# Performance work log

Measured on AMD Instinct MI355X. Metric: run time of the kernel, lower is better.

The kernel has to match this reference:

```python
import jax, jax.numpy as jnp
import numpy as np

B, T, C, H = 2, 2048, 1024, 16
D = C // H  # head_dim = 64

def setup_inputs() -> dict:
    key = jax.random.key(0)
    ks = jax.random.split(key, 9)
    s = 1.0 / np.sqrt(C)
    return {
        "x": jax.random.normal(ks[0], (B, T, C), dtype=jnp.float32),
        "Wq": jax.random.uniform(ks[1], (C, C), jnp.float32, -s, s),
        "bq": jax.random.uniform(ks[2], (C,), jnp.float32, -s, s),
        "Wk": jax.random.uniform(ks[3], (C, C), jnp.float32, -s, s),
        "bk": jax.random.uniform(ks[4], (C,), jnp.float32, -s, s),
        "Wv": jax.random.uniform(ks[5], (C, C), jnp.float32, -s, s),
        "bv": jax.random.uniform(ks[6], (C,), jnp.float32, -s, s),
        "Wp": jax.random.uniform(ks[7], (C, C), jnp.float32, -s, s),
        "bp": jax.random.uniform(ks[8], (C,), jnp.float32, -s, s),
    }

def reference(x, Wq, bq, Wk, bk, Wv, bv, Wp, bp):
    # Linear layers: torch nn.Linear weight is [out,in], so x @ W.T + b
    q = x @ Wq.T + bq
    k = x @ Wk.T + bk
    v = x @ Wv.T + bv
    # [B,T,C] -> [B,H,T,D]
    q = q.reshape(B, T, H, D).transpose(0, 2, 1, 3)
    k = k.reshape(B, T, H, D).transpose(0, 2, 1, 3)
    v = v.reshape(B, T, H, D).transpose(0, 2, 1, 3)
    att = jnp.einsum("bhqd,bhkd->bhqk", q, k) / jnp.sqrt(jnp.float32(D))
    causal = jnp.tril(jnp.ones((T, T), dtype=bool))  # [T,T]
    att = jnp.where(causal, att, jnp.float32(-jnp.inf))
    att = jax.nn.softmax(att, axis=-1)
    out = jnp.einsum("bhqk,bhkd->bhqd", att, v)
    out = out.transpose(0, 2, 1, 3).reshape(B, T, C)
    return out @ Wp.T + bp
```

## Files before the change

kernel.cpp:

```cpp
#include <hip/hip_runtime.h>
#include <hip/hip_bf16.h>
#include <stdint.h>

typedef __bf16 bf16x8 __attribute__((ext_vector_type(8)));
typedef __bf16 bf16x4 __attribute__((ext_vector_type(4)));
typedef __bf16 bf16x2 __attribute__((ext_vector_type(2)));
typedef float  f32x4  __attribute__((ext_vector_type(4)));
typedef float  f32x16v __attribute__((ext_vector_type(16)));

#define MFMA16(A,B,Cc) __builtin_amdgcn_mfma_f32_16x16x32_bf16(A,B,Cc,0,0,0)
#define MFMA32(A,B,Cc) __builtin_amdgcn_mfma_f32_32x32x16_bf16(A,B,Cc,0,0,0)

__device__ inline unsigned pack2(float a, float b) {
  union { bf16x2 v; unsigned u; } t;
  t.v[0] = (__bf16)a; t.v[1] = (__bf16)b;
  return t.u;
}
__device__ inline bf16x8 frag4(unsigned w0, unsigned w1, unsigned w2, unsigned w3) {
  union { unsigned u[4]; bf16x8 v; } t;
  t.u[0] = w0; t.u[1] = w1; t.u[2] = w2; t.u[3] = w3;
  return t.v;
}

__device__ inline void pswap(unsigned& a, unsigned& b) {
#if __has_builtin(__builtin_amdgcn_permlane32_swap)
  auto r = __builtin_amdgcn_permlane32_swap(a, b, false, false);
  a = r[0]; b = r[1];
#else
  asm volatile("v_permlane32_swap_b32 %0, %1" : "+v"(a), "+v"(b));
#endif
}
__device__ inline float cross32_sum(float v) {
  unsigned a = __builtin_bit_cast(unsigned, v), b = a;
  pswap(a, b);
  return __builtin_bit_cast(float, a) + __builtin_bit_cast(float, b);
}

__device__ inline void gl16(const __bf16* g, __bf16* l) {
  __builtin_amdgcn_global_load_lds(
      (const __attribute__((address_space(1))) void*)(uintptr_t)g,
      (__attribute__((address_space(3))) void*)(uintptr_t)l, 16, 0, 0);
}

__global__ __launch_bounds__(256) void conv_kernel(
    const float* __restrict__ x,
    const float* __restrict__ Wq, const float* __restrict__ Wk,
    const float* __restrict__ Wv, const float* __restrict__ Wp,
    __bf16* __restrict__ xb, __bf16* __restrict__ Wb)
{
  const int z = blockIdx.y;
  const float* src;
  __bf16* dst;
  int n4;
  if (z == 0) { src = x;  dst = xb; n4 = 1048576; }
  else {
    src = (z == 1) ? Wq : (z == 2) ? Wk : (z == 3) ? Wv : Wp;
    dst = Wb + (size_t)(z - 1) * 1048576;
    n4  = 262144;
  }
  const f32x4* s4 = (const f32x4*)src;
  for (int i = blockIdx.x * 256 + threadIdx.x; i < n4; i += gridDim.x * 256) {
    const f32x4 v = s4[i];
    bf16x4 o;
#pragma unroll
    for (int j = 0; j < 4; ++j) o[j] = (__bf16)v[j];
    *(bf16x4*)(dst + (size_t)i * 4) = o;
  }
}

__device__ inline void gemm_core(const __bf16* __restrict__ A,
                                 const __bf16* __restrict__ W,
                                 int m0, int n0,
                                 __bf16* As, __bf16* Bs,
                                 f32x4 (&acc)[4][4])
{
  const int tid = threadIdx.x, lane = tid & 63;
  const int wid = tid >> 6, wr = wid >> 1, wc = wid & 1;
  const int g = lane >> 4, cl = lane & 15;
  const int sr = tid >> 2, sk = (tid & 3) * 8;
  __bf16* AsW = As + (tid & 192) * 8;
  __bf16* BsW = Bs + (tid & 192) * 8;

  for (int k0 = 0; k0 < 1024; k0 += 32) {
    __syncthreads();
    gl16(A + (size_t)(m0 + sr)      * 1024 + k0 + sk, AsW);
    gl16(A + (size_t)(m0 + sr + 64) * 1024 + k0 + sk, AsW + 2048);
    gl16(W + (size_t)(n0 + sr)      * 1024 + k0 + sk, BsW);
    gl16(W + (size_t)(n0 + sr + 64) * 1024 + k0 + sk, BsW + 2048);
    __syncthreads();
    bf16x8 af[4], bfr[4];
#pragma unroll
    for (int m = 0; m < 4; ++m)
      af[m] = *(const bf16x8*)(As + (wr * 64 + m * 16 + cl) * 32 + g * 8);
#pragma unroll
    for (int n = 0; n < 4; ++n)
      bfr[n] = *(const bf16x8*)(Bs + (wc * 64 + n * 16 + cl) * 32 + g * 8);
#pragma unroll
    for (int m = 0; m < 4; ++m)
#pragma unroll
      for (int n = 0; n < 4; ++n)
        acc[m][n] = MFMA16(af[m], bfr[n], acc[m][n]);
  }
}

__global__ __launch_bounds__(256) void gemm_qkv128(
    const __bf16* __restrict__ xb, const __bf16* __restrict__ Wb,
    const float* __restrict__ bq, const float* __restrict__ bk,
    const float* __restrict__ bv,
    __bf16* __restrict__ Qw, __bf16* __restrict__ Kw, __bf16* __restrict__ Vw)
{
  __shared__ __align__(16) __bf16 As[128 * 32];
  __shared__ __align__(16) __bf16 Bs[128 * 32];

  const int orig = blockIdx.x;
  const int wg   = (orig & 7) * 96 + (orig >> 3);
  const int z    = wg >> 8;
  const int rem  = wg & 255;
  const int m0   = (rem >> 3) * 128;
  const int n0   = (rem & 7) * 128;

  const __bf16* W  = Wb + (size_t)z * 1048576;
  const float*  bi = (z == 0) ? bq : (z == 1) ? bk : bv;
  __bf16*       out = (z == 0) ? Qw : (z == 1) ? Kw : Vw;

  f32x4 acc[4][4] = {};
  gemm_core(xb, W, m0, n0, As, Bs, acc);

  const int lane = threadIdx.x & 63, wid = threadIdx.x >> 6;
  const int wr = wid >> 1, wc = wid & 1;
  const int g = lane >> 4, cl = lane & 15;

  float bvv[4];
#pragma unroll
  for (int n = 0; n < 4; ++n) bvv[n] = bi[n0 + wc * 64 + n * 16 + cl];

#pragma unroll
  for (int m = 0; m < 4; ++m)
#pragma unroll
    for (int n = 0; n < 4; ++n) {
      const int col = n0 + wc * 64 + n * 16 + cl;
      const int h = col >> 6, d = col & 63;
      if (z == 2) {
        const int row0 = m0 + wr * 64 + m * 16 + g * 4;
        const int b2 = row0 >> 11, t0 = row0 & 2047;
        bf16x4 v4;
#pragma unroll
        for (int j = 0; j < 4; ++j) v4[j] = (__bf16)(acc[m][n][j] + bvv[n]);
        *(bf16x4*)(out + (size_t)(b2 * 16 + h) * 131072 + (size_t)d * 2048 + t0) = v4;
      } else {
#pragma unroll
        for (int j = 0; j < 4; ++j) {
          const int row = m0 + wr * 64 + m * 16 + g * 4 + j;
          const int b2 = row >> 11, t = row & 2047;
          out[(size_t)(b2 * 16 + h) * 131072 + (size_t)t * 64 + d] =
              (__bf16)(acc[m][n][j] + bvv[n]);
        }
      }
    }
}

__global__ __launch_bounds__(256) void gemm_proj128(
    const __bf16* __restrict__ A, const __bf16* __restrict__ W,
    const float* __restrict__ bi, float* __restrict__ outp)
{
  __shared__ __align__(16) __bf16 As[128 * 32];
  __shared__ __align__(16) __bf16 Bs[128 * 32];

  const int orig = blockIdx.x;
  const int wg   = (orig & 7) * 32 + (orig >> 3);
  const int m0   = (wg >> 3) * 128;
  const int n0   = (wg & 7) * 128;

  f32x4 acc[4][4] = {};
  gemm_core(A, W, m0, n0, As, Bs, acc);

  const int lane = threadIdx.x & 63, wid = threadIdx.x >> 6;
  const int wr = wid >> 1, wc = wid & 1;
  const int g = lane >> 4, cl = lane & 15;

  float bvv[4];
#pragma unroll
  for (int n = 0; n < 4; ++n) bvv[n] = bi[n0 + wc * 64 + n * 16 + cl];
#pragma unroll
  for (int m = 0; m < 4; ++m)
#pragma unroll
    for (int n = 0; n < 4; ++n) {
      const int col = n0 + wc * 64 + n * 16 + cl;
#pragma unroll
      for (int j = 0; j < 4; ++j) {
        const int row = m0 + wr * 64 + m * 16 + g * 4 + j;
        outp[(size_t)row * 1024 + col] = acc[m][n][j] + bvv[n];
      }
    }
}

__device__ inline void attn_tile(
    const __bf16* __restrict__ Kb, const __bf16* __restrict__ vrow0,
    const __bf16* __restrict__ vrow1, const bf16x8 (&qf)[4],
    int kv0, bool diag, int l31, int hi,
    float& L, f32x16v& o0, f32x16v& o1)
{
  const float SC = 0.18033688f;
  const float CSH = 2.0f;

  const bf16x8 kf0 = *(const bf16x8*)(Kb + (kv0 + l31) * 64 +      hi * 8);
  const bf16x8 kf1 = *(const bf16x8*)(Kb + (kv0 + l31) * 64 + 16 + hi * 8);
  const bf16x8 kf2 = *(const bf16x8*)(Kb + (kv0 + l31) * 64 + 32 + hi * 8);
  const bf16x8 kf3 = *(const bf16x8*)(Kb + (kv0 + l31) * 64 + 48 + hi * 8);
  const bf16x8 va0 = *(const bf16x8*)(vrow0 + kv0 + hi * 8);
  const bf16x8 va1 = *(const bf16x8*)(vrow1 + kv0 + hi * 8);
  const bf16x8 va2 = *(const bf16x8*)(vrow0 + kv0 + 16 + hi * 8);
  const bf16x8 va3 = *(const bf16x8*)(vrow1 + kv0 + 16 + hi * 8);

  f32x16v s = {};
  s = MFMA32(kf0, qf[0], s);
  s = MFMA32(kf1, qf[1], s);
  s = MFMA32(kf2, qf[2], s);
  s = MFMA32(kf3, qf[3], s);

  if (diag) {
#pragma unroll
    for (int r = 0; r < 16; ++r) {
      const int kl = (r & 3) + 8 * (r >> 2) + 4 * hi;
      if (kl > l31) s[r] = -1e30f;
    }
  }
  float pr[16];
#pragma unroll
  for (int r = 0; r < 16; ++r)
    pr[r] = exp2f(__builtin_fmaf(s[r], SC, -CSH));
  {
    float t0 = (pr[0] + pr[1])   + (pr[2] + pr[3]);
    float t1 = (pr[4] + pr[5])   + (pr[6] + pr[7]);
    float t2 = (pr[8] + pr[9])   + (pr[10] + pr[11]);
    float t3 = (pr[12] + pr[13]) + (pr[14] + pr[15]);
    L += cross32_sum((t0 + t1) + (t2 + t3));
  }

  unsigned c0 = pack2(pr[0],  pr[1]),  c1 = pack2(pr[2],  pr[3]);
  unsigned c2 = pack2(pr[4],  pr[5]),  c3 = pack2(pr[6],  pr[7]);
  unsigned c4 = pack2(pr[8],  pr[9]),  c5 = pack2(pr[10], pr[11]);
  unsigned c6 = pack2(pr[12], pr[13]), c7 = pack2(pr[14], pr[15]);
  pswap(c0, c2);
  pswap(c1, c3);
  pswap(c4, c6);
  pswap(c5, c7);
  const bf16x8 pf0 = frag4(c0, c1, c2, c3);
  const bf16x8 pf1 = frag4(c4, c5, c6, c7);

  o0 = MFMA32(va0, pf0, o0);
  o1 = MFMA32(va1, pf0, o1);
  o0 = MFMA32(va2, pf1, o0);
  o1 = MFMA32(va3, pf1, o1);
}

__global__ __launch_bounds__(256, 4) void attn_kernel(
    const __bf16* __restrict__ Q, const __bf16* __restrict__ K,
    const __bf16* __restrict__ Vt, __bf16* __restrict__ Oc)
{
  const int bh  = blockIdx.x;
  const int p   = blockIdx.y;
  const int w   = threadIdx.x >> 6;
  const int lane = threadIdx.x & 63;
  const int l31 = lane & 31, hi = lane >> 5;

  const __bf16* Qb = Q  + (size_t)bh * 131072;
  const __bf16* Kb = K  + (size_t)bh * 131072;
  const __bf16* Vb = Vt + (size_t)bh * 131072;
  const __bf16* vrow0 = Vb + (size_t)l31 * 2048;
  const __bf16* vrow1 = Vb + (size_t)(32 + l31) * 2048;

  __shared__ __bf16 SO[8][64][36];
  __shared__ float  SL[8][64];

  const int qsS[2] = { p * 32, (63 - p) * 32 };
  const int nS[2]  = { p + 1, 64 - p };

#pragma unroll
  for (int ph = 0; ph < 2; ++ph) {
    const int qs = qsS[ph], nT = nS[ph];
    bf16x8 qf[4];
#pragma unroll
    for (int c = 0; c < 4; ++c)
      qf[c] = *(const bf16x8*)(Qb + (qs + l31) * 64 + c * 16 + hi * 8);

    f32x16v o0 = {}, o1 = {};
    float L = 0.f;

    for (int t = w; t < nT; t += 4)
      attn_tile(Kb, vrow0, vrow1, qf, t * 32, t == nT - 1, l31, hi,
                L, o0, o1);

    const int slot = ph * 4 + w;
#pragma unroll
    for (int q4 = 0; q4 < 4; ++q4) {
      bf16x4 a, b;
#pragma unroll
      for (int j = 0; j < 4; ++j) {
        a[j] = (__bf16)o0[q4 * 4 + j];
        b[j] = (__bf16)o1[q4 * 4 + j];
      }
      *(bf16x4*)&SO[slot][lane][q4 * 4]      = a;
      *(bf16x4*)&SO[slot][lane][16 + q4 * 4] = b;
    }
    SL[slot][lane] = L;
  }

  __syncthreads();
  if (w < 2) {
    const int base = w * 4;
    const int qs = qsS[w];
    const float Lt = SL[base][lane] + SL[base + 1][lane] +
                     SL[base + 2][lane] + SL[base + 3][lane];
    const float inv = 1.0f / Lt;

    const int b = bh >> 4, h = bh & 15;
    const int tq = qs + l31;
    __bf16* orow = Oc + (size_t)(b * 2048 + tq) * 1024 + h * 64;
#pragma unroll
    for (int q4 = 0; q4 < 4; ++q4) {
      bf16x4 v0, v1;
      float acc0[4] = {}, acc1[4] = {};
#pragma unroll
      for (int s = 0; s < 4; ++s) {
        const bf16x4 a4 = *(const bf16x4*)&SO[base + s][lane][q4 * 4];
        const bf16x4 b4 = *(const bf16x4*)&SO[base + s][lane][16 + q4 * 4];
#pragma unroll
        for (int j = 0; j < 4; ++j) {
          acc0[j] += (float)a4[j];
          acc1[j] += (float)b4[j];
        }
      }
#pragma unroll
      for (int j = 0; j < 4; ++j) {
        v0[j] = (__bf16)(acc0[j] * inv);
        v1[j] = (__bf16)(acc1[j] * inv);
      }
      const int d0 = 8 * q4 + 4 * hi;
      *(bf16x4*)(orow + d0)      = v0;
      *(bf16x4*)(orow + 32 + d0) = v1;
    }
  }
}

extern "C" void kernel_launch(void* const* d_in, const int* in_sizes, int n_in,
                              void* d_out, int out_size, void* d_ws, size_t ws_size,
                              hipStream_t stream) {
  const float* x  = (const float*)d_in[0];
  const float* Wq = (const float*)d_in[1];
  const float* bq = (const float*)d_in[2];
  const float* Wk = (const float*)d_in[3];
  const float* bk = (const float*)d_in[4];
  const float* Wv = (const float*)d_in[5];
  const float* bv = (const float*)d_in[6];
  const float* Wp = (const float*)d_in[7];
  const float* bp = (const float*)d_in[8];

  __bf16* Qw  = (__bf16*)d_ws;
  __bf16* Kw  = Qw + (size_t)4194304;
  __bf16* Vw  = Kw + (size_t)4194304;
  __bf16* xbA = Vw + (size_t)4194304;
  __bf16* Wb  = xbA + (size_t)4194304;

  conv_kernel<<<dim3(512, 5), 256, 0, stream>>>(x, Wq, Wk, Wv, Wp, xbA, Wb);
  gemm_qkv128<<<768, 256, 0, stream>>>(xbA, Wb, bq, bk, bv, Qw, Kw, Vw);
  attn_kernel<<<dim3(32, 32), 256, 0, stream>>>(Qw, Kw, Vw, xbA );
  gemm_proj128<<<256, 256, 0, stream>>>(xbA , Wb + (size_t)3 * 1048576,
                                        bp, (float*)d_out);
}
```

Measured before the change: 134.8 us.

## Fuse the two causal query phases into one KV loop sharing K/V loads

The kernel previously ran the paired query blocks (early and late in the causal triangle) as two separate passes over the key/value tiles, loading K and V twice. It now walks the KV tiles once and, for tiles both blocks need, computes scores and PV for both query blocks from the same loaded fragments. This halves global K/V loads for the shared prefix and gives the MFMA units more independent work per iteration. The cost is higher register pressure from two sets of Q fragments and accumulators, which could lower occupancy under the 256x4 launch bounds.

```diff
diff --git a/kernel.cpp b/kernel.cpp
--- a/kernel.cpp
+++ b/kernel.cpp
@@ -194,37 +194,21 @@
     }
 }
 
-__device__ inline void attn_tile(
-    const __bf16* __restrict__ Kb, const __bf16* __restrict__ vrow0,
-    const __bf16* __restrict__ vrow1, const bf16x8 (&qf)[4],
-    int kv0, bool diag, int l31, int hi,
-    float& L, f32x16v& o0, f32x16v& o1)
+__device__ inline void mask_diag(f32x16v& s, int l31, int hi) {
+#pragma unroll
+  for (int r = 0; r < 16; ++r) {
+    const int kl = (r & 3) + 8 * (r >> 2) + 4 * hi;
+    if (kl > l31) s[r] = -1e30f;
+  }
+}
+
+__device__ inline void soft_pv(const f32x16v& s, float& L,
+                               f32x16v& o0, f32x16v& o1,
+                               const bf16x8& va0, const bf16x8& va1,
+                               const bf16x8& va2, const bf16x8& va3)
 {
   const float SC = 0.18033688f;
   const float CSH = 2.0f;
-
-  const bf16x8 kf0 = *(const bf16x8*)(Kb + (kv0 + l31) * 64 +      hi * 8);
-  const bf16x8 kf1 = *(const bf16x8*)(Kb + (kv0 + l31) * 64 + 16 + hi * 8);
-  const bf16x8 kf2 = *(const bf16x8*)(Kb + (kv0 + l31) * 64 + 32 + hi * 8);
-  const bf16x8 kf3 = *(const bf16x8*)(Kb + (kv0 + l31) * 64 + 48 + hi * 8);
-  const bf16x8 va0 = *(const bf16x8*)(vrow0 + kv0 + hi * 8);
-  const bf16x8 va1 = *(const bf16x8*)(vrow1 + kv0 + hi * 8);
-  const bf16x8 va2 = *(const bf16x8*)(vrow0 + kv0 + 16 + hi * 8);
-  const bf16x8 va3 = *(const bf16x8*)(vrow1 + kv0 + 16 + hi * 8);
-
-  f32x16v s = {};
-  s = MFMA32(kf0, qf[0], s);
-  s = MFMA32(kf1, qf[1], s);
-  s = MFMA32(kf2, qf[2], s);
-  s = MFMA32(kf3, qf[3], s);
-
-  if (diag) {
-#pragma unroll
-    for (int r = 0; r < 16; ++r) {
-      const int kl = (r & 3) + 8 * (r >> 2) + 4 * hi;
-      if (kl > l31) s[r] = -1e30f;
-    }
-  }
   float pr[16];
 #pragma unroll
   for (int r = 0; r < 16; ++r)
@@ -236,7 +220,6 @@
     float t3 = (pr[12] + pr[13]) + (pr[14] + pr[15]);
     L += cross32_sum((t0 + t1) + (t2 + t3));
   }
-
   unsigned c0 = pack2(pr[0],  pr[1]),  c1 = pack2(pr[2],  pr[3]);
   unsigned c2 = pack2(pr[4],  pr[5]),  c3 = pack2(pr[6],  pr[7]);
   unsigned c4 = pack2(pr[8],  pr[9]),  c5 = pack2(pr[10], pr[11]);
@@ -247,7 +230,6 @@
   pswap(c5, c7);
   const bf16x8 pf0 = frag4(c0, c1, c2, c3);
   const bf16x8 pf1 = frag4(c4, c5, c6, c7);
-
   o0 = MFMA32(va0, pf0, o0);
   o1 = MFMA32(va1, pf0, o1);
   o0 = MFMA32(va2, pf1, o0);
@@ -273,24 +255,55 @@
   __shared__ __bf16 SO[8][64][36];
   __shared__ float  SL[8][64];
 
-  const int qsS[2] = { p * 32, (63 - p) * 32 };
-  const int nS[2]  = { p + 1, 64 - p };
+  const int qsA = p * 32, qsB = (63 - p) * 32;
+  const int nA  = p + 1,  nB  = 64 - p;
+
+  bf16x8 qfA[4], qfB[4];
+#pragma unroll
+  for (int c = 0; c < 4; ++c) {
+    qfA[c] = *(const bf16x8*)(Qb + (qsA + l31) * 64 + c * 16 + hi * 8);
+    qfB[c] = *(const bf16x8*)(Qb + (qsB + l31) * 64 + c * 16 + hi * 8);
+  }
+
+  f32x16v oA0 = {}, oA1 = {}, oB0 = {}, oB1 = {};
+  float LA = 0.f, LB = 0.f;
+
+  for (int t = w; t < nB; t += 4) {
+    const int kv0 = t * 32;
+    const bf16x8 kf0 = *(const bf16x8*)(Kb + (kv0 + l31) * 64 +      hi * 8);
+    const bf16x8 kf1 = *(const bf16x8*)(Kb + (kv0 + l31) * 64 + 16 + hi * 8);
+    const bf16x8 kf2 = *(const bf16x8*)(Kb + (kv0 + l31) * 64 + 32 + hi * 8);
+    const bf16x8 kf3 = *(const bf16x8*)(Kb + (kv0 + l31) * 64 + 48 + hi * 8);
+    const bf16x8 va0 = *(const bf16x8*)(vrow0 + kv0 + hi * 8);
+    const bf16x8 va1 = *(const bf16x8*)(vrow1 + kv0 + hi * 8);
+    const bf16x8 va2 = *(const bf16x8*)(vrow0 + kv0 + 16 + hi * 8);
+    const bf16x8 va3 = *(const bf16x8*)(vrow1 + kv0 + 16 + hi * 8);
+
+    if (t < nA) {
+      f32x16v sA = {}, sB = {};
+      sA = MFMA32(kf0, qfA[0], sA);  sB = MFMA32(kf0, qfB[0], sB);
+      sA = MFMA32(kf1, qfA[1], sA);  sB = MFMA32(kf1, qfB[1], sB);
+      sA = MFMA32(kf2, qfA[2], sA);  sB = MFMA32(kf2, qfB[2], sB);
+      sA = MFMA32(kf3, qfA[3], sA);  sB = MFMA32(kf3, qfB[3], sB);
+      if (t == nA - 1) mask_diag(sA, l31, hi);
+      if (t == nB - 1) mask_diag(sB, l31, hi);
+      soft_pv(sA, LA, oA0, oA1, va0, va1, va2, va3);
+      soft_pv(sB, LB, oB0, oB1, va0, va1, va2, va3);
+    } else {
+      f32x16v sB = {};
+      sB = MFMA32(kf0, qfB[0], sB);
+      sB = MFMA32(kf1, qfB[1], sB);
+      sB = MFMA32(kf2, qfB[2], sB);
+      sB = MFMA32(kf3, qfB[3], sB);
+      if (t == nB - 1) mask_diag(sB, l31, hi);
+      soft_pv(sB, LB, oB0, oB1, va0, va1, va2, va3);
+    }
+  }
 
 #pragma unroll
   for (int ph = 0; ph < 2; ++ph) {
-    const int qs = qsS[ph], nT = nS[ph];
-    bf16x8 qf[4];
-#pragma unroll
-    for (int c = 0; c < 4; ++c)
-      qf[c] = *(const bf16x8*)(Qb + (qs + l31) * 64 + c * 16 + hi * 8);
-
-    f32x16v o0 = {}, o1 = {};
-    float L = 0.f;
-
-    for (int t = w; t < nT; t += 4)
-      attn_tile(Kb, vrow0, vrow1, qf, t * 32, t == nT - 1, l31, hi,
-                L, o0, o1);
-
+    const f32x16v& o0 = ph ? oB0 : oA0;
+    const f32x16v& o1 = ph ? oB1 : oA1;
     const int slot = ph * 4 + w;
 #pragma unroll
     for (int q4 = 0; q4 < 4; ++q4) {
@@ -303,13 +316,13 @@
       *(bf16x4*)&SO[slot][lane][q4 * 4]      = a;
       *(bf16x4*)&SO[slot][lane][16 + q4 * 4] = b;
     }
-    SL[slot][lane] = L;
+    SL[slot][lane] = ph ? LB : LA;
   }
 
   __syncthreads();
   if (w < 2) {
     const int base = w * 4;
-    const int qs = qsS[w];
+    const int qs = w ? qsB : qsA;
     const float Lt = SL[base][lane] + SL[base + 1][lane] +
                      SL[base + 2][lane] + SL[base + 3][lane];
     const float inv = 1.0f / Lt;
```

After: 194.8 us. 44.5% more time.
